# Performance work log

Hardware: AMD Instinct MI355X
Metric: run time of the kernel (lower is better)

The kernel has to match this reference:

```python
import jax, jax.numpy as jnp
import numpy as np

B, IN, H = 4096, 1024, 1024


def setup_inputs() -> dict:
    key = jax.random.key(0)
    ks = jax.random.split(key, 6)
    s_h = 1.0 / np.sqrt(H)
    s_x = 1.0 / np.sqrt(IN)
    return {
        "x": jax.random.normal(ks[0], (B, IN), jnp.float32),
        "h": jax.random.normal(ks[1], (B, H), jnp.float32),
        "c": jax.random.normal(ks[2], (B, H), jnp.float32),
        # hidden_lin: Linear(H, 4H) with bias
        "Wh": jax.random.uniform(ks[3], (4 * H, H), jnp.float32, -s_h, s_h),
        "bh": jax.random.uniform(ks[4], (4 * H,), jnp.float32, -s_h, s_h),
        # input_lin: Linear(IN, 4H), bias=False
        "Wx": jax.random.uniform(ks[5], (4 * H, IN), jnp.float32, -s_x, s_x),
    }


def reference(x, h, c, Wh, bh, Wx):
    # ifgo = h @ Wh^T + bh + x @ Wx^T   -> [B, 4H]
    ifgo = jnp.dot(h, Wh.T) + bh + jnp.dot(x, Wx.T)
    i, f, g, o = jnp.split(ifgo, 4, axis=1)
    i = jax.nn.sigmoid(i)
    f = jax.nn.sigmoid(f)
    g = jnp.tanh(g)
    o = jax.nn.sigmoid(o)
    c_next = f * c + i * g
    h_next = o * jnp.tanh(c_next)
    return (h_next, c_next)
```

## Files before the change

kernel.cpp:

```cpp
#include <hip/hip_runtime.h>
#include <cstdint>
#include <cstddef>


#define NB   4096
#define KH   1024
#define KK   2048
#define ARR_ELEMS 4194304
#define NKT  32

typedef __bf16 bf16x8 __attribute__((ext_vector_type(8)));
typedef float  f32x4  __attribute__((ext_vector_type(4)));

__device__ inline unsigned short f2bf(float f) {
    union { float f; unsigned int u; } v; v.f = f;
    unsigned int u = v.u;
    u += 0x7FFFu + ((u >> 16) & 1u);
    return (unsigned short)(u >> 16);
}

__device__ inline float fsig(float v)  { return __builtin_amdgcn_rcpf(1.f + __expf(-v)); }
__device__ inline float ftanh(float v) { return 1.f - 2.f * __builtin_amdgcn_rcpf(1.f + __expf(2.f * v)); }

__global__ void convert_kernel(const float* __restrict__ h, const float* __restrict__ x,
                               const float* __restrict__ Wh, const float* __restrict__ Wx,
                               unsigned short* __restrict__ A, unsigned short* __restrict__ W) {
    int idx = blockIdx.x * 256 + threadIdx.x;
    int arr = idx >> 19;
    int off = (idx & 0x7FFFF) << 3;
    const float* src = (arr == 0) ? h : (arr == 1) ? x : (arr == 2) ? Wh : Wx;
    float4 v0 = *(const float4*)(src + off);
    float4 v1 = *(const float4*)(src + off + 4);
    uint4 packed;
    packed.x = (unsigned int)f2bf(v0.x) | ((unsigned int)f2bf(v0.y) << 16);
    packed.y = (unsigned int)f2bf(v0.z) | ((unsigned int)f2bf(v0.w) << 16);
    packed.z = (unsigned int)f2bf(v1.x) | ((unsigned int)f2bf(v1.y) << 16);
    packed.w = (unsigned int)f2bf(v1.z) | ((unsigned int)f2bf(v1.w) << 16);

    int row = off >> 10;
    int col = off & 1023;
    unsigned short* dst;
    size_t dstOff;
    if (arr < 2) {
        dst = A;
        dstOff = (size_t)row * KK + (arr == 1 ? 1024 : 0) + col;
    } else {
        int g = row >> 10, j = row & 1023;
        int p = ((j >> 4) << 6) | (g << 4) | (j & 15);
        dst = W;
        dstOff = (size_t)p * KK + (arr == 3 ? 1024 : 0) + col;
    }
    *(uint4*)(dst + dstOff) = packed;
}

__global__ __launch_bounds__(512, 2) void gemm_kernel(const unsigned short* __restrict__ A,
                            const unsigned short* __restrict__ W,
                            const float* __restrict__ bh,
                            const float* __restrict__ c,
                            float* __restrict__ out) {
    __shared__ __align__(16) unsigned short As[2 * 16384];
    __shared__ __align__(16) unsigned short Bs[2 * 16384];

    const int tid  = threadIdx.x;
    const int wave = tid >> 6;
    const int lane = tid & 63;

    const int bid   = (int)blockIdx.x;
    const int swz   = (bid & 7) * 32 + (bid >> 3);
    const int tileM = swz >> 4;
    const int tileN = swz & 15;

    const int wr  = wave >> 2;
    const int wc  = wave & 3;
    const int fr  = lane & 15;
    const int fk2 = (lane >> 4) << 4;

    const unsigned short* pa[4];
    const unsigned short* pb[4];
    #pragma unroll
    for (int i = 0; i < 4; ++i) {
        const int P   = (i * 512 + tid) * 16;
        const int L   = P ^ (((P >> 7) & 7) << 4);
        const int row = L >> 7;
        const int kk  = (L & 127) >> 1;
        pa[i] = A + (size_t)(tileM * 256 + row) * KK + kk;
        pb[i] = W + (size_t)(tileN * 256 + row) * KK + kk;
    }

    const int swzm = (fr & 7) << 4;
    int offA[8], offB[4];
    #pragma unroll
    for (int i = 0; i < 8; ++i)
        offA[i] = (wr * 128 + i * 16 + fr) * 128 + (fk2 ^ swzm);
    #pragma unroll
    for (int j = 0; j < 4; ++j)
        offB[j] = (wc * 64 + j * 16 + fr) * 128 + (fk2 ^ swzm);

    f32x4 acc[8][4] = {};
    bf16x8 a03[4][2], a47[4][2], b01[2][2], b23[2][2];

#define STAGE(KT, BUF) do { \
    const size_t _ko = (size_t)(KT) * 64; \
    _Pragma("unroll") \
    for (int _i = 0; _i < 4; ++_i) { \
        __builtin_amdgcn_global_load_lds( \
            (const __attribute__((address_space(1))) void*)(pa[_i] + _ko), \
            (__attribute__((address_space(3))) void*)(As + (BUF) * 16384 + _i * 4096 + wave * 512), 16, 0, 0); \
        __builtin_amdgcn_global_load_lds( \
            (const __attribute__((address_space(1))) void*)(pb[_i] + _ko), \
            (__attribute__((address_space(3))) void*)(Bs + (BUF) * 16384 + _i * 4096 + wave * 512), 16, 0, 0); \
    } \
} while (0)

#define READ_A(dst, base, AsB) do { \
    _Pragma("unroll") \
    for (int _i = 0; _i < 4; ++_i) { \
        dst[_i][0] = *(const bf16x8*)((AsB) + offA[(base) + _i]); \
        dst[_i][1] = *(const bf16x8*)((AsB) + (offA[(base) + _i] ^ 64)); \
    } \
} while (0)

#define READ_B(dst, base, BsB) do { \
    _Pragma("unroll") \
    for (int _j = 0; _j < 2; ++_j) { \
        dst[_j][0] = *(const bf16x8*)((BsB) + offB[(base) + _j]); \
        dst[_j][1] = *(const bf16x8*)((BsB) + (offB[(base) + _j] ^ 64)); \
    } \
} while (0)

#define MFMAQ(af, bf, IB, JB) do { \
    __builtin_amdgcn_s_setprio(1); \
    _Pragma("unroll") \
    for (int _i = 0; _i < 4; ++_i) \
        _Pragma("unroll") \
        for (int _j = 0; _j < 2; ++_j) \
            _Pragma("unroll") \
            for (int _s = 0; _s < 2; ++_s) \
                acc[(IB) + _i][(JB) + _j] = __builtin_amdgcn_mfma_f32_16x16x32_bf16( \
                    af[_i][_s], bf[_j][_s], acc[(IB) + _i][(JB) + _j], 0, 0, 0); \
    __builtin_amdgcn_s_setprio(0); \
} while (0)

#define TILEBODY(T, BUF) do { \
    const char* AsB = (const char*)As + (BUF) * 32768; \
    const char* BsB = (const char*)Bs + (BUF) * 32768; \
    READ_B(b01, 0, BsB); \
    READ_A(a03, 0, AsB); \
    READ_A(a47, 4, AsB); \
    MFMAQ(a03, b01, 0, 0); \
    READ_B(b23, 2, BsB); \
    MFMAQ(a47, b01, 4, 0); \
    MFMAQ(a47, b23, 4, 2); \
    asm volatile("s_waitcnt lgkmcnt(0)" ::: "memory"); \
    asm volatile("s_barrier" ::: "memory"); \
    { \
        const int _kt = ((T) + 2 <= NKT - 1) ? ((T) + 2) : (NKT - 1); \
        STAGE(_kt, BUF);    \
    } \
    asm volatile("s_waitcnt vmcnt(8)" ::: "memory"); \
    asm volatile("s_barrier" ::: "memory"); \
    MFMAQ(a03, b23, 0, 2); \
} while (0)

    STAGE(0, 0);
    STAGE(1, 1);
    asm volatile("s_waitcnt vmcnt(8)" ::: "memory");
    asm volatile("s_barrier" ::: "memory");

    for (int tt = 0; tt < NKT; tt += 2) {
        TILEBODY(tt, 0);
        TILEBODY(tt + 1, 1);
    }
#undef TILEBODY
#undef MFMAQ
#undef READ_A
#undef READ_B
#undef STAGE

    const int j = ((tileN * 4 + wc) << 4) | fr;
    const float bi  = bh[j];
    const float bff = bh[j + 1024];
    const float bg  = bh[j + 2048];
    const float bo  = bh[j + 3072];

    const int row0 = tileM * 256 + wr * 128 + (lane >> 4) * 4;

    float cv[8][4];
    #pragma unroll
    for (int i = 0; i < 8; ++i)
        #pragma unroll
        for (int r = 0; r < 4; ++r)
            cv[i][r] = c[(size_t)(row0 + i * 16 + r) * KH + j];

    #pragma unroll
    for (int i = 0; i < 8; ++i) {
        #pragma unroll
        for (int r = 0; r < 4; ++r) {
            const size_t idx = (size_t)(row0 + i * 16 + r) * KH + j;
            float iv = fsig(acc[i][0][r] + bi);
            float fv = fsig(acc[i][1][r] + bff);
            float gv = ftanh(acc[i][2][r] + bg);
            float ov = fsig(acc[i][3][r] + bo);
            float cn = fv * cv[i][r] + iv * gv;
            float hn = ov * ftanh(cn);
            out[idx] = hn;
            out[(size_t)ARR_ELEMS + idx] = cn;
        }
    }
}

extern "C" void kernel_launch(void* const* d_in, const int* in_sizes, int n_in,
                              void* d_out, int out_size, void* d_ws, size_t ws_size,
                              hipStream_t stream) {
    const float* x  = (const float*)d_in[0];
    const float* h  = (const float*)d_in[1];
    const float* c  = (const float*)d_in[2];
    const float* Wh = (const float*)d_in[3];
    const float* bh = (const float*)d_in[4];
    const float* Wx = (const float*)d_in[5];
    float* out = (float*)d_out;

    unsigned short* ws   = (unsigned short*)d_ws;
    unsigned short* Acat = ws;
    unsigned short* Wcat = ws + 2 * (size_t)ARR_ELEMS;

    convert_kernel<<<8192, 256, 0, stream>>>(h, x, Wh, Wx, Acat, Wcat);
    gemm_kernel<<<256, 512, 0, stream>>>(Acat, Wcat, bh, c, out);
}
```

Before: 194.8 us.

## Restructure GEMM main loop into four-phase pipeline with triple-buffered B tile

Splits each K-tile iteration into four MFMA quarters, each interleaved with an LDS fragment read for the next quarter and a partial global-to-LDS prefetch, separated by waitcnt+barrier clumps. B gets a third LDS buffer so the next tile's B fragments can be read before the current buffer is overwritten, and A fragments for the next tile are preloaded across the iteration boundary. The aim is to hide LDS-read and global-load latency behind MFMAs instead of having one large sync point per tile. In exchange it uses more LDS, which may limit the two-blocks-per-CU occupancy, and it adds four barriers per tile.

Result: slower. 216.7 us (+11.3%).

```diff
diff --git a/kernel.cpp b/kernel.cpp
--- a/kernel.cpp
+++ b/kernel.cpp
@@ -59,7 +59,7 @@
                             const float* __restrict__ c,
                             float* __restrict__ out) {
     __shared__ __align__(16) unsigned short As[2 * 16384];
-    __shared__ __align__(16) unsigned short Bs[2 * 16384];
+    __shared__ __align__(16) unsigned short Bs[3 * 16384];
 
     const int tid  = threadIdx.x;
     const int wave = tid >> 6;
@@ -97,18 +97,25 @@
         offB[j] = (wc * 64 + j * 16 + fr) * 128 + (fk2 ^ swzm);
 
     f32x4 acc[8][4] = {};
-    bf16x8 a03[4][2], a47[4][2], b01[2][2], b23[2][2];
-
-#define STAGE(KT, BUF) do { \
+    bf16x8 a03[4][2], a47[4][2], b23[2][2], b01A[2][2], b01B[2][2];
+
+#define STAGE_B_H(H, KT, BUF) do { \
     const size_t _ko = (size_t)(KT) * 64; \
     _Pragma("unroll") \
-    for (int _i = 0; _i < 4; ++_i) { \
+    for (int _i = 2*(H); _i < 2*(H)+2; ++_i) \
+        __builtin_amdgcn_global_load_lds( \
+            (const __attribute__((address_space(1))) void*)(pb[_i] + _ko), \
+            (__attribute__((address_space(3))) void*)(Bs + (BUF) * 16384 + _i * 4096 + wave * 512), 16, 0, 0); \
+} while (0)
+
+#define STAGE_A_Q(Q, KT, BUF) do { \
+    const size_t _ko = (size_t)(KT) * 64; \
+    _Pragma("unroll") \
+    for (int _k = 0; _k < 2; ++_k) { \
+        const int _i = (Q) + 2 * _k;    \
         __builtin_amdgcn_global_load_lds( \
             (const __attribute__((address_space(1))) void*)(pa[_i] + _ko), \
             (__attribute__((address_space(3))) void*)(As + (BUF) * 16384 + _i * 4096 + wave * 512), 16, 0, 0); \
-        __builtin_amdgcn_global_load_lds( \
-            (const __attribute__((address_space(1))) void*)(pb[_i] + _ko), \
-            (__attribute__((address_space(3))) void*)(Bs + (BUF) * 16384 + _i * 4096 + wave * 512), 16, 0, 0); \
     } \
 } while (0)
 
@@ -139,43 +146,68 @@
                 acc[(IB) + _i][(JB) + _j] = __builtin_amdgcn_mfma_f32_16x16x32_bf16( \
                     af[_i][_s], bf[_j][_s], acc[(IB) + _i][(JB) + _j], 0, 0, 0); \
     __builtin_amdgcn_s_setprio(0); \
-} while (0)
-
-#define TILEBODY(T, BUF) do { \
-    const char* AsB = (const char*)As + (BUF) * 32768; \
-    const char* BsB = (const char*)Bs + (BUF) * 32768; \
-    READ_B(b01, 0, BsB); \
-    READ_A(a03, 0, AsB); \
-    READ_A(a47, 4, AsB); \
-    MFMAQ(a03, b01, 0, 0); \
-    READ_B(b23, 2, BsB); \
-    MFMAQ(a47, b01, 4, 0); \
+    __builtin_amdgcn_sched_barrier(0); \
+} while (0)
+
+#define CLUMP do { \
+    asm volatile("s_waitcnt vmcnt(6) lgkmcnt(0)" ::: "memory"); \
+    __builtin_amdgcn_s_barrier(); \
+} while (0)
+
+#define TILEBODY(T, AB, BB, ABn, BBn, BBs, bcur, bnxt) do { \
+    const char* AsT = (const char*)As + (AB) * 32768; \
+    const char* AsN = (const char*)As + (ABn) * 32768; \
+    const char* BsT = (const char*)Bs + (BB) * 32768; \
+    const char* BsN = (const char*)Bs + (BBn) * 32768; \
+    const int _t2 = ((T) + 2 <= NKT - 1) ? ((T) + 2) : (NKT - 1); \
+     \
+    MFMAQ(a03, bcur, 0, 0); \
+    READ_B(b23, 2, BsT); \
+    STAGE_B_H(0, _t2, BBs); \
+    CLUMP; \
+     \
+    MFMAQ(a03, b23, 0, 2); \
+    READ_A(a47, 4, AsT); \
+    STAGE_B_H(1, _t2, BBs); \
+    CLUMP; \
+     \
     MFMAQ(a47, b23, 4, 2); \
-    asm volatile("s_waitcnt lgkmcnt(0)" ::: "memory"); \
-    asm volatile("s_barrier" ::: "memory"); \
-    { \
-        const int _kt = ((T) + 2 <= NKT - 1) ? ((T) + 2) : (NKT - 1); \
-        STAGE(_kt, BUF);    \
-    } \
-    asm volatile("s_waitcnt vmcnt(8)" ::: "memory"); \
-    asm volatile("s_barrier" ::: "memory"); \
-    MFMAQ(a03, b23, 0, 2); \
-} while (0)
-
-    STAGE(0, 0);
-    STAGE(1, 1);
+    READ_A(a03, 0, AsN); \
+    STAGE_A_Q(0, _t2, AB); \
+    CLUMP; \
+     \
+    MFMAQ(a47, bcur, 4, 0); \
+    READ_B(bnxt, 0, BsN); \
+    STAGE_A_Q(1, _t2, AB); \
+    CLUMP; \
+} while (0)
+
+    STAGE_B_H(0, 0, 0); STAGE_B_H(1, 0, 0);
+    STAGE_A_Q(0, 0, 0); STAGE_A_Q(1, 0, 0);
+    STAGE_B_H(0, 1, 1); STAGE_B_H(1, 1, 1);
+    STAGE_A_Q(0, 1, 1); STAGE_A_Q(1, 1, 1);
     asm volatile("s_waitcnt vmcnt(8)" ::: "memory");
-    asm volatile("s_barrier" ::: "memory");
-
-    for (int tt = 0; tt < NKT; tt += 2) {
-        TILEBODY(tt, 0);
-        TILEBODY(tt + 1, 1);
-    }
+    __builtin_amdgcn_s_barrier();
+    READ_A(a03, 0, (const char*)As);
+    READ_B(b01A, 0, (const char*)Bs);
+
+    for (int tt = 0; tt < 30; tt += 6) {
+        TILEBODY(tt + 0, 0, 0, 1, 1, 2, b01A, b01B);
+        TILEBODY(tt + 1, 1, 1, 0, 2, 0, b01B, b01A);
+        TILEBODY(tt + 2, 0, 2, 1, 0, 1, b01A, b01B);
+        TILEBODY(tt + 3, 1, 0, 0, 1, 2, b01B, b01A);
+        TILEBODY(tt + 4, 0, 1, 1, 2, 0, b01A, b01B);
+        TILEBODY(tt + 5, 1, 2, 0, 0, 1, b01B, b01A);
+    }
+    TILEBODY(30, 0, 0, 1, 1, 2, b01A, b01B);
+    TILEBODY(31, 1, 1, 0, 2, 0, b01B, b01A);
 #undef TILEBODY
+#undef CLUMP
 #undef MFMAQ
 #undef READ_A
 #undef READ_B
-#undef STAGE
+#undef STAGE_A_Q
+#undef STAGE_B_H
 
     const int j = ((tileN * 4 + wc) << 4) | fr;
     const float bi  = bh[j];
```
